# Kernel tuning notes

Hardware: AMD Instinct MI355X
Metric: run time of the kernel (lower is better)

## Reference

```python
import jax, jax.numpy as jnp
import numpy as np

H, KV, D, HID = 32, 2, 128, 4096
SQ, SMAX, CP, L = 1024, 4096, 3072, 4
LAYER_IDX = 0


def setup_inputs() -> dict:
    key = jax.random.key(0)
    ks = jax.random.split(key, 14)
    hidden_states = jax.random.normal(ks[0], (1, HID, 1, SQ), jnp.float32)
    # RoPE tables (values in [-1,1]; layout per forward: cos/sin act on last dim of K,
    # cos_t/sin_t are the transposed tables acting on dim -2 of Q)
    cos = jax.random.uniform(ks[1], (1, 1, SQ, D), jnp.float32, -1.0, 1.0)
    sin = jax.random.uniform(ks[2], (1, 1, SQ, D), jnp.float32, -1.0, 1.0)
    cos_t = jax.random.uniform(ks[3], (1, 1, D, SQ), jnp.float32, -1.0, 1.0)
    sin_t = jax.random.uniform(ks[4], (1, 1, D, SQ), jnp.float32, -1.0, 1.0)
    # causal mask in (kv_pos, q_pos) layout: query q sits at absolute position CP+q
    kv_pos = jnp.arange(SMAX)[:, None]
    q_pos = jnp.arange(SQ)[None, :]
    attention_mask = jnp.where(kv_pos <= CP + q_pos, 0.0, -1e9).astype(jnp.float32)[None, None]
    key_cache = jax.random.normal(ks[5], (L, KV, SMAX, D), jnp.float32)
    value_cache = jax.random.normal(ks[6], (L, KV, SMAX, D), jnp.float32)
    s = 0.02
    wq = jax.random.normal(ks[7], (H * D, HID), jnp.float32) * s
    bq = jax.random.normal(ks[8], (H * D,), jnp.float32) * s
    wk = jax.random.normal(ks[9], (KV * D, HID), jnp.float32) * s
    bk = jax.random.normal(ks[10], (KV * D,), jnp.float32) * s
    wv = jax.random.normal(ks[11], (KV * D, HID), jnp.float32) * s
    bv = jax.random.normal(ks[12], (KV * D,), jnp.float32) * s
    wo = jax.random.normal(ks[13], (HID, H * D), jnp.float32) * s
    return dict(hidden_states=hidden_states, cos=cos, sin=sin, cos_t=cos_t, sin_t=sin_t,
                attention_mask=attention_mask, key_cache=key_cache, value_cache=value_cache,
                wq=wq, bq=bq, wk=wk, bk=bk, wv=wv, bv=bv, wo=wo, cache_position=CP)


def _rotate_half(x, axis):
    x1, x2 = jnp.split(x, 2, axis=axis)
    return jnp.concatenate([-x2, x1], axis=axis)


def reference(hidden_states, cos, sin, cos_t, sin_t, attention_mask,
              key_cache, value_cache, wq, bq, wk, bk, wv, bv, wo, cache_position):
    cp = int(cache_position)
    # 1x1-conv projections == matmul over channel dim; hidden_states (1, HID, 1, SQ)
    q = jnp.einsum('oi,bihs->bohs', wq, hidden_states) + bq[None, :, None, None]
    k = jnp.einsum('oi,bihs->bohs', wk, hidden_states) + bk[None, :, None, None]
    v = jnp.einsum('oi,bihs->bohs', wv, hidden_states) + bv[None, :, None, None]
    q = q.reshape(1, H, D, SQ)                      # (1, H, D, Sq)
    k = k.reshape(1, KV, D, SQ).swapaxes(2, 3)      # (1, KV, Sq, D)
    v = v.reshape(1, KV, D, SQ).swapaxes(2, 3)      # (1, KV, Sq, D)
    # split-half RoPE: q rotated along dim -2 (head_dim axis), k along dim -1
    q = q * cos_t + _rotate_half(q, -2) * sin_t
    k = k * cos + _rotate_half(k, -1) * sin
    # scatter into KV cache at [layer_idx, :, cp:cp+SQ]
    kc = key_cache.at[LAYER_IDX, :, cp:cp + SQ, :].set(k[0])
    vc = value_cache.at[LAYER_IDX, :, cp:cp + SQ, :].set(v[0])
    kl = kc[LAYER_IDX]   # (KV, Smax, D)
    vl = vc[LAYER_IDX]   # (KV, Smax, D)
    qg = q.reshape(KV, H // KV, D, SQ)  # group G=H/KV query heads per kv head
    # K @ Q per kv-head group, softmax over kv positions (axis=2)
    attn = jnp.einsum('ksd,kgdq->kgsq', kl, qg) / jnp.sqrt(jnp.float32(D))
    attn = attn + attention_mask[0]     # broadcast (1, Smax, Sq) over (KV, G, Smax, Sq)
    attn = jax.nn.softmax(attn, axis=2)
    out = jnp.einsum('kgsq,ksd->kgqd', attn, vl)    # (KV, G, Sq, D)
    out = out.reshape(1, H, SQ, D).swapaxes(2, 3).reshape(1, H * D, 1, SQ)
    out = jnp.einsum('oi,bihs->bohs', wo, out)      # (1, HID, 1, Sq)
    return out
```

## Files before the change

### kernel.cpp

```cpp
#include <hip/hip_runtime.h>
#include <stdint.h>

#define H_    32
#define KV_   2
#define D_    128
#define HID_  4096
#define SQ_   1024
#define SMAX_ 4096

typedef unsigned short u16;
typedef __attribute__((ext_vector_type(8))) short bf16x8;
typedef __attribute__((ext_vector_type(8))) unsigned short u16x8;
typedef __attribute__((ext_vector_type(4))) float f32x4;

#define MFMA16(a, b, c) __builtin_amdgcn_mfma_f32_16x16x32_bf16(a, b, c, 0, 0, 0)

__device__ __forceinline__ u16 f2bf(float f) {
  unsigned u = __float_as_uint(f);
  u += 0x7fffu + ((u >> 16) & 1u);
  return (u16)(u >> 16);
}
__device__ __forceinline__ float bf2f(u16 u) {
  return __uint_as_float(((unsigned)u) << 16);
}
__device__ __forceinline__ float exp2_fast(float x) {
  float r;
  asm("v_exp_f32 %0, %1" : "=v"(r) : "v"(x));
  return r;
}
__device__ __forceinline__ unsigned cvt_pk_bf16(float lo, float hi) {
  unsigned r;
  asm("v_cvt_pk_bf16_f32 %0, %1, %2" : "=v"(r) : "v"(lo), "v"(hi));
  return r;
}

__device__ __forceinline__ void gl_lds16(const void* g, void* l) {
  __builtin_amdgcn_global_load_lds(
      (const __attribute__((address_space(1))) unsigned int*)g,
      (__attribute__((address_space(3))) unsigned int*)l, 16, 0, 0);
}

__global__ __launch_bounds__(256) void k_ht(const float* __restrict__ hs,
                                            u16* __restrict__ ht) {
  __shared__ float tl[64][65];
  const int i0 = blockIdx.x << 6, s0 = blockIdx.y << 6;
  const int tid = threadIdx.x;
  {
    const int r = tid >> 2, c = (tid & 3) << 4;
    const float* p = hs + (i0 + r) * SQ_ + s0 + c;
    float4 a = *(const float4*)p;
    float4 b = *(const float4*)(p + 4);
    float4 cc = *(const float4*)(p + 8);
    float4 d = *(const float4*)(p + 12);
    float* q = &tl[r][c];
    q[0] = a.x; q[1] = a.y; q[2] = a.z; q[3] = a.w;
    q[4] = b.x; q[5] = b.y; q[6] = b.z; q[7] = b.w;
    q[8] = cc.x; q[9] = cc.y; q[10] = cc.z; q[11] = cc.w;
    q[12] = d.x; q[13] = d.y; q[14] = d.z; q[15] = d.w;
  }
  __syncthreads();
  {
    const int sr = tid >> 2, c = (tid & 3) << 4;
    u16x8 o0, o1;
#pragma unroll
    for (int j = 0; j < 8; ++j) o0[j] = f2bf(tl[c + j][sr]);
#pragma unroll
    for (int j = 0; j < 8; ++j) o1[j] = f2bf(tl[c + 8 + j][sr]);
    u16* q = ht + (s0 + sr) * HID_ + i0 + c;
    *(u16x8*)q = o0;
    *(u16x8*)(q + 8) = o1;
  }
}

__global__ __launch_bounds__(256) void k_wconv4(const float* __restrict__ s0,
                                                const float* __restrict__ s1,
                                                const float* __restrict__ s2,
                                                const float* __restrict__ s3,
                                                u16* __restrict__ dbase) {
  const int N0 = (H_ * D_ * HID_) / 8;
  const int N1 = (KV_ * D_ * HID_) / 8;
  const int NT = N0 + 2 * N1 + N0;
  const int stride = gridDim.x << 8;
  for (int i = (blockIdx.x << 8) + threadIdx.x; i < NT; i += stride) {
    const float* s;
    int j;
    if (i < N0) { s = s0; j = i; }
    else if (i < N0 + N1) { s = s1; j = i - N0; }
    else if (i < N0 + 2 * N1) { s = s2; j = i - N0 - N1; }
    else { s = s3; j = i - N0 - 2 * N1; }
    const float4 a = ((const float4*)s)[2 * j];
    const float4 b = ((const float4*)s)[2 * j + 1];
    u16x8 o;
    o[0] = f2bf(a.x); o[1] = f2bf(a.y); o[2] = f2bf(a.z); o[3] = f2bf(a.w);
    o[4] = f2bf(b.x); o[5] = f2bf(b.y); o[6] = f2bf(b.z); o[7] = f2bf(b.w);
    ((u16x8*)dbase)[i] = o;
  }
}

template <int OUTMODE, bool SWZ>
__global__ __launch_bounds__(256, 2) void k_gemm_bf(const u16* __restrict__ A,
                                                    const float* __restrict__ bias,
                                                    const u16* __restrict__ B,
                                                    void* __restrict__ Cout,
                                                    const int* __restrict__ cpp,
                                                    int ldc,
                                                    const float* __restrict__ bk2,
                                                    const float* __restrict__ bv2,
                                                    u16* __restrict__ knr2,
                                                    u16* __restrict__ vt2) {
  __shared__ u16 a_t[2][64 * 64];
  __shared__ u16 b_t[2][128 * 64];
  int nx, my;
  if (SWZ) {
    const int bid = blockIdx.x;
    const int xcd = bid & 7, t = bid >> 3;
    nx = t & 7;
    my = ((t >> 3) << 3) | xcd;
  } else {
    nx = blockIdx.x;
    my = blockIdx.y;
  }
  const int n0 = nx << 7, m0 = my << 6;
  const int tid = threadIdx.x, wid = tid >> 6, lane = tid & 63;
  const int l15 = lane & 15, l4 = lane >> 4;
  const int wn = wid << 5;
  const f32x4 z4 = {0.f, 0.f, 0.f, 0.f};
  f32x4 acc[4][2];
#pragma unroll
  for (int i = 0; i < 4; ++i)
#pragma unroll
    for (int j = 0; j < 2; ++j) acc[i][j] = z4;

  const int lr8 = lane >> 3, sl = lane & 7;
  const char* sp[6];
  u16* dp[6];
  int stp[6];
#pragma unroll
  for (int j = 0; j < 6; ++j) {
    const int L = wid * 6 + j;
    const bool isA = (L < 8);
    const int Lr = isA ? L : (L - 8);
    const int row = (Lr << 3) + lr8;
    const int cs = sl ^ (row & 7);
    const size_t grow = isA ? (size_t)(m0 + row) : (size_t)(n0 + row);
    sp[j] = (const char*)((isA ? A : B) + grow * HID_) + (cs << 4);
    dp[j] = (isA ? &a_t[0][0] : &b_t[0][0]) + (Lr << 9);
    stp[j] = isA ? 4096 : 8192;
  }
#define GSTAGE(buf, kt)                                     \
  {                                                         \
    _Pragma("unroll") for (int j = 0; j < 6; ++j)           \
        gl_lds16(sp[j] + ((size_t)(kt) << 7),               \
                 dp[j] + ((buf) ? stp[j] : 0));             \
  }

  GSTAGE(0, 0);
  __syncthreads();
  int cur = 0;
  for (int kt = 0; kt < HID_ / 64; ++kt) {
    if (kt + 1 < HID_ / 64) GSTAGE(cur ^ 1, kt + 1);
#pragma unroll
    for (int kk = 0; kk < 2; ++kk) {
      bf16x8 af[4], bfr[2];
#pragma unroll
      for (int mf = 0; mf < 4; ++mf) {
        const int row = mf * 16 + l15;
        const int slt = ((kk << 2) + l4) ^ (row & 7);
        af[mf] = *(const bf16x8*)((const char*)&a_t[cur][0] + (row << 7) + (slt << 4));
      }
#pragma unroll
      for (int nf = 0; nf < 2; ++nf) {
        const int row = wn + nf * 16 + l15;
        const int slt = ((kk << 2) + l4) ^ (row & 7);
        bfr[nf] = *(const bf16x8*)((const char*)&b_t[cur][0] + (row << 7) + (slt << 4));
      }
#pragma unroll
      for (int nf = 0; nf < 2; ++nf)
#pragma unroll
        for (int mf = 0; mf < 4; ++mf) acc[mf][nf] = MFMA16(af[mf], bfr[nf], acc[mf][nf]);
    }
    __syncthreads();
    cur ^= 1;
  }
#undef GSTAGE

  if (OUTMODE == 3) {
    const int cp = cpp[0];
#pragma unroll
    for (int mf = 0; mf < 4; ++mf) {
#pragma unroll
      for (int r = 0; r < 4; ++r) {
        const int m = m0 + mf * 16 + (l4 << 2) + r;
        float bi;
        u16* dst;
        if (m < 4096) { bi = bias[m]; dst = (u16*)Cout + (size_t)m * SQ_; }
        else if (m < 4352) { bi = bk2[m - 4096]; dst = knr2 + (size_t)(m - 4096) * SQ_; }
        else { bi = bv2[m - 4352]; dst = vt2 + (size_t)(m - 4352) * SMAX_ + cp; }
#pragma unroll
        for (int nf = 0; nf < 2; ++nf) {
          const int n = n0 + wn + nf * 16 + l15;
          dst[n] = f2bf(acc[mf][nf][r] + bi);
        }
      }
    }
  } else {
#pragma unroll
    for (int mf = 0; mf < 4; ++mf) {
#pragma unroll
      for (int r = 0; r < 4; ++r) {
        const int m = m0 + mf * 16 + (l4 << 2) + r;
        const float bi = bias ? bias[m] : 0.f;
#pragma unroll
        for (int nf = 0; nf < 2; ++nf) {
          const int n = n0 + wn + nf * 16 + l15;
          const float v = acc[mf][nf][r] + bi;
          if (OUTMODE == 2)
            ((float*)Cout)[(size_t)m * ldc + n] = v;
          else
            ((u16*)Cout)[(size_t)m * ldc + n] = f2bf(v);
        }
      }
    }
  }
}

template <int OUTMODE>
__global__ __launch_bounds__(256) void k_gemm_f32A(const float* __restrict__ A,
                                                   const float* __restrict__ bias,
                                                   const u16* __restrict__ B,
                                                   void* __restrict__ Cout,
                                                   const int* __restrict__ cpp,
                                                   int ldc) {
  __shared__ u16 a_t[128 * 32];
  __shared__ u16 b_t[128 * 32];
  const int n0 = blockIdx.x << 7, m0 = blockIdx.y << 7;
  const int tid = threadIdx.x;
  const int wid = tid >> 6, lane = tid & 63;
  const int l15 = lane & 15, l4 = lane >> 4;
  const int wm = (wid >> 1) * 64, wn = (wid & 1) * 64;
  const f32x4 z4 = {0.f, 0.f, 0.f, 0.f};
  f32x4 acc[4][4];
#pragma unroll
  for (int i = 0; i < 4; ++i)
#pragma unroll
    for (int j = 0; j < 4; ++j) acc[i][j] = z4;
  const int arow = tid >> 1, ac = (tid & 1) << 4;
  const float* Ap = A + (size_t)(m0 + arow) * HID_ + ac;
  const u16* Bp = B + (size_t)(n0 + arow) * HID_ + ac;
  for (int kt = 0; kt < HID_ / 32; ++kt) {
    float4 f0 = *(const float4*)(Ap);
    float4 f1 = *(const float4*)(Ap + 4);
    float4 f2 = *(const float4*)(Ap + 8);
    float4 f3 = *(const float4*)(Ap + 12);
    uint4 b0 = *(const uint4*)(Bp);
    uint4 b1 = *(const uint4*)(Bp + 8);
    Ap += 32;
    Bp += 32;
    u16x8 ua0, ua1;
    ua0[0] = f2bf(f0.x); ua0[1] = f2bf(f0.y); ua0[2] = f2bf(f0.z); ua0[3] = f2bf(f0.w);
    ua0[4] = f2bf(f1.x); ua0[5] = f2bf(f1.y); ua0[6] = f2bf(f1.z); ua0[7] = f2bf(f1.w);
    ua1[0] = f2bf(f2.x); ua1[1] = f2bf(f2.y); ua1[2] = f2bf(f2.z); ua1[3] = f2bf(f2.w);
    ua1[4] = f2bf(f3.x); ua1[5] = f2bf(f3.y); ua1[6] = f2bf(f3.z); ua1[7] = f2bf(f3.w);
    __syncthreads();
    *(u16x8*)&a_t[arow * 32 + ac] = ua0;
    *(u16x8*)&a_t[arow * 32 + ac + 8] = ua1;
    *(uint4*)&b_t[arow * 32 + ac] = b0;
    *(uint4*)&b_t[arow * 32 + ac + 8] = b1;
    __syncthreads();
    bf16x8 af[4];
#pragma unroll
    for (int mf = 0; mf < 4; ++mf)
      af[mf] = *(const bf16x8*)&a_t[(wm + mf * 16 + l15) * 32 + l4 * 8];
#pragma unroll
    for (int nf = 0; nf < 4; ++nf) {
      bf16x8 bfr = *(const bf16x8*)&b_t[(wn + nf * 16 + l15) * 32 + l4 * 8];
#pragma unroll
      for (int mf = 0; mf < 4; ++mf) acc[mf][nf] = MFMA16(af[mf], bfr, acc[mf][nf]);
    }
  }
  const int coff = (OUTMODE == 1) ? cpp[0] : 0;
#pragma unroll
  for (int mf = 0; mf < 4; ++mf) {
#pragma unroll
    for (int r = 0; r < 4; ++r) {
      const int m = m0 + wm + mf * 16 + l4 * 4 + r;
      const float bi = bias ? bias[m] : 0.f;
#pragma unroll
      for (int nf = 0; nf < 4; ++nf) {
        const int n = n0 + wn + nf * 16 + l15;
        const float v = acc[mf][nf][r] + bi;
        if (OUTMODE == 2)
          ((float*)Cout)[(size_t)m * ldc + n] = v;
        else
          ((u16*)Cout)[(size_t)m * ldc + n + coff] = f2bf(v);
      }
    }
  }
}

__global__ __launch_bounds__(256) void k_rope_q(const u16* __restrict__ qnr,
                                                const float* __restrict__ cost,
                                                const float* __restrict__ sint,
                                                u16* __restrict__ Qr) {
  __shared__ u16 qt[128 * 64];
  __shared__ float ct[128 * 64];
  __shared__ float st[128 * 64];
  const int s0 = blockIdx.x << 6, h = blockIdx.y;
  const int tid = threadIdx.x;
  {
    const int r = tid >> 1, c = (tid & 1) << 5;
    const u16* p = qnr + (h * 128 + r) * SQ_ + s0 + c;
#pragma unroll
    for (int j = 0; j < 4; ++j) *(uint4*)&qt[r * 64 + c + j * 8] = *(const uint4*)(p + j * 8);
    const float* cpr = cost + r * SQ_ + s0 + c;
    const float* spr = sint + r * SQ_ + s0 + c;
#pragma unroll
    for (int j = 0; j < 8; ++j) {
      *(float4*)&ct[r * 64 + c + j * 4] = *(const float4*)(cpr + j * 4);
      *(float4*)&st[r * 64 + c + j * 4] = *(const float4*)(spr + j * 4);
    }
  }
  __syncthreads();
  const int sl = tid >> 2, d0 = (tid & 3) << 5;
  u16* op = Qr + (((h << 10) + s0 + sl) << 7) + d0;
#pragma unroll
  for (int g = 0; g < 4; ++g) {
    u16x8 o;
#pragma unroll
    for (int j = 0; j < 8; ++j) {
      const int d = d0 + g * 8 + j;
      const float v = bf2f(qt[d * 64 + sl]);
      const float vp = bf2f(qt[(d ^ 64) * 64 + sl]);
      const float sgn = (d < 64) ? -1.f : 1.f;
      o[j] = f2bf(v * ct[d * 64 + sl] + sgn * vp * st[d * 64 + sl]);
    }
    *(u16x8*)(op + g * 8) = o;
  }
}

__global__ __launch_bounds__(256) void k_rope_k(const u16* __restrict__ knr,
                                                const float* __restrict__ cosp,
                                                const float* __restrict__ sinp,
                                                const int* __restrict__ cpp,
                                                u16* __restrict__ kful) {
  __shared__ u16 kt_[128 * 64];
  const int s0 = blockIdx.x << 6, kk = blockIdx.y;
  const int cp = cpp[0];
  const int tid = threadIdx.x;
  {
    const int r = tid >> 1, c = (tid & 1) << 5;
    const u16* p = knr + (kk * 128 + r) * SQ_ + s0 + c;
#pragma unroll
    for (int j = 0; j < 4; ++j) *(uint4*)&kt_[r * 64 + c + j * 8] = *(const uint4*)(p + j * 8);
  }
  __syncthreads();
  const int sl = tid >> 2, d0 = (tid & 3) << 5;
  const int s = s0 + sl;
  const float* crow = cosp + s * D_;
  const float* srow = sinp + s * D_;
  u16* op = kful + ((kk * SMAX_ + cp + s) << 7) + d0;
#pragma unroll
  for (int g = 0; g < 4; ++g) {
    u16x8 o;
#pragma unroll
    for (int j = 0; j < 8; ++j) {
      const int d = d0 + g * 8 + j;
      const float v = bf2f(kt_[d * 64 + sl]);
      const float vp = bf2f(kt_[(d ^ 64) * 64 + sl]);
      const float sgn = (d < 64) ? -1.f : 1.f;
      o[j] = f2bf(v * crow[d] + sgn * vp * srow[d]);
    }
    *(u16x8*)(op + g * 8) = o;
  }
}

__global__ __launch_bounds__(256) void k_prefk(const float* __restrict__ kc,
                                               const int* __restrict__ cpp,
                                               u16* __restrict__ kful) {
  const int cp = cpp[0];
  const int idx = (blockIdx.x << 8) + threadIdx.x;
  const int base = idx << 3;
  const int s = (base >> 7) & (SMAX_ - 1);
  if (s >= cp) return;
  const float* p = kc + base;
  float4 a = *(const float4*)p;
  float4 b = *(const float4*)(p + 4);
  u16x8 o;
  o[0] = f2bf(a.x); o[1] = f2bf(a.y); o[2] = f2bf(a.z); o[3] = f2bf(a.w);
  o[4] = f2bf(b.x); o[5] = f2bf(b.y); o[6] = f2bf(b.z); o[7] = f2bf(b.w);
  *(u16x8*)(kful + base) = o;
}

__global__ __launch_bounds__(256) void k_prefvt(const float* __restrict__ vc,
                                                const int* __restrict__ cpp,
                                                u16* __restrict__ vt) {
  const int cp = cpp[0];
  const int s0 = blockIdx.x << 6, d0 = blockIdx.y << 6, kk = blockIdx.z;
  if (s0 >= cp) return;
  __shared__ float tl[64][65];
  const int tid = threadIdx.x;
  {
    const int r = tid >> 2, c = (tid & 3) << 4;
    if (s0 + r < cp) {
      const float* p = vc + ((kk * SMAX_ + s0 + r) << 7) + d0 + c;
#pragma unroll
      for (int j = 0; j < 4; ++j) {
        float4 v = *(const float4*)(p + j * 4);
        tl[r][c + j * 4 + 0] = v.x;
        tl[r][c + j * 4 + 1] = v.y;
        tl[r][c + j * 4 + 2] = v.z;
        tl[r][c + j * 4 + 3] = v.w;
      }
    }
  }
  __syncthreads();
  const int dl = tid >> 2, c = (tid & 3) << 4;
  u16* op = vt + (kk * D_ + d0 + dl) * SMAX_ + s0 + c;
  if (s0 + c + 15 < cp) {
    u16x8 o0, o1;
#pragma unroll
    for (int j = 0; j < 8; ++j) o0[j] = f2bf(tl[c + j][dl]);
#pragma unroll
    for (int j = 0; j < 8; ++j) o1[j] = f2bf(tl[c + 8 + j][dl]);
    *(u16x8*)op = o0;
    *(u16x8*)(op + 8) = o1;
  } else {
#pragma unroll
    for (int j = 0; j < 16; ++j)
      if (s0 + c + j < cp) op[j] = f2bf(tl[c + j][dl]);
  }
}

__device__ __forceinline__ void attn_stageK8(const char* KfB, int kv0, u16* kbuf,
                                             int wid, int lane) {
  const int kcb = (lane & 15) << 4;
#pragma unroll
  for (int j = 0; j < 2; ++j) {
    const int L = (wid << 1) + j;
    const int row = (L << 2) + (lane >> 4);
    gl_lds16(KfB + (((size_t)(kv0 + row)) << 8) + (kcb ^ ((row & 7) << 4)),
             kbuf + (L << 9));
  }
}
__device__ __forceinline__ void attn_stageV8(const char* VtB, int kv0, u16* vbuf,
                                             int wid, int lane) {
  const int vcb = (lane & 7) << 4;
#pragma unroll
  for (int j = 0; j < 2; ++j) {
    const int L = (wid << 1) + j;
    const int row = (L << 3) + (lane >> 3);
    gl_lds16(VtB + ((((size_t)row * SMAX_) + kv0) << 1) + (vcb ^ ((row & 7) << 4)),
             vbuf + (L << 9));
  }
}

template <int SPLIT>
__global__ __launch_bounds__(512, 4) void k_attn(const u16* __restrict__ Q,
                                                 const u16* __restrict__ Kf,
                                                 const u16* __restrict__ Vt,
                                                 const int* __restrict__ cpp,
                                                 u16* __restrict__ Ob,
                                                 float* __restrict__ Opart,
                                                 float* __restrict__ Ml) {
  __shared__ u16 Kb[2][8192];
  __shared__ u16 Vb[2][8192];
  __shared__ u16 Pl[8][1024];
  int h, qb, ch;
  if (SPLIT) {
    const int bid = blockIdx.x;
    const int xcd = bid & 7, s = bid >> 3;
    h = ((xcd >> 2) << 4) | (xcd & 3) | ((s & 3) << 2);
    qb = (s >> 2) & 7;
    ch = s >> 5;
  } else {
    h = blockIdx.x;
    qb = blockIdx.y;
    ch = 0;
  }
  const int cp = cpp[0];
  const int kk = h >> 4;
  const int tid = threadIdx.x, wid = tid >> 6, lane = tid & 63;
  const int l15 = lane & 15, l4 = lane >> 4;
  const int qrow_base = (qb << 7) + (wid << 4);
  char* pl = (char*)&Pl[wid][0];

  bf16x8 aq[4];
#pragma unroll
  for (int ks = 0; ks < 4; ++ks)
    aq[ks] = *(const bf16x8*)&Q[(((size_t)(h << 10) + qrow_base + l15) << 7) + ks * 32 + (l4 << 3)];

  const f32x4 z4 = {0.f, 0.f, 0.f, 0.f};
  f32x4 oacc[8];
  float mrun = -1e30f, lrun = 0.f;
#pragma unroll
  for (int nf = 0; nf < 8; ++nf) oacc[nf] = z4;

  const int ntf0 = ((cp + (qb << 7) + 127) >> 6) + 1;
  const int ntf = ntf0 < (SMAX_ >> 6) ? ntf0 : (SMAX_ >> 6);
  const int t0 = (SPLIT && ch) ? 32 : 0;
  const int t1 = (SPLIT && !ch) ? 32 : ntf;
  const float SC2 = 0.12751879523568785f;

  const char* KfB = (const char*)Kf + ((size_t)kk * SMAX_ << 8);
  const char* VtB = (const char*)Vt + ((size_t)kk << 20);

  attn_stageK8(KfB, t0 << 6, Kb[0], wid, lane);
  attn_stageV8(VtB, t0 << 6, Vb[0], wid, lane);
  __syncthreads();
  int cur = 0;

  for (int kt = t0; kt < t1; ++kt) {
    const int kv0 = kt << 6;
    if (kt + 1 < t1) {
      attn_stageK8(KfB, kv0 + 64, Kb[cur ^ 1], wid, lane);
      attn_stageV8(VtB, kv0 + 64, Vb[cur ^ 1], wid, lane);
    }
    const char* kb = (const char*)Kb[cur];
    const char* vb = (const char*)Vb[cur];
    f32x4 sa[4];
#pragma unroll
    for (int nf = 0; nf < 4; ++nf) sa[nf] = z4;
#pragma unroll
    for (int ks = 0; ks < 4; ++ks) {
#pragma unroll
      for (int nf = 0; nf < 4; ++nf) {
        const int rk = nf * 16 + l15;
        bf16x8 bk = *(const bf16x8*)(kb + (((rk << 8) + (ks << 6) + (l4 << 4)) ^ ((rk & 7) << 4)));
        sa[nf] = MFMA16(bk, aq[ks], sa[nf]);
      }
    }
    const int lim = cp + qrow_base + l15;
    const bool needmask = (kv0 + 63) > (cp + qrow_base);
    float x[4][4];
#pragma unroll
    for (int nf = 0; nf < 4; ++nf)
#pragma unroll
      for (int r = 0; r < 4; ++r) {
        float v = sa[nf][r] * SC2;
        if (needmask && (kv0 + nf * 16 + (l4 << 2) + r > lim)) v = -1e9f;
        x[nf][r] = v;
      }
    float ml = x[0][0];
#pragma unroll
    for (int nf = 0; nf < 4; ++nf)
#pragma unroll
      for (int r = 0; r < 4; ++r) ml = fmaxf(ml, x[nf][r]);
    ml = fmaxf(ml, __shfl_xor(ml, 16));
    ml = fmaxf(ml, __shfl_xor(ml, 32));
    const bool need = !__all(ml <= mrun + 11.54f);
    const float mnew = need ? fmaxf(ml, mrun) : mrun;
    float rs = 0.f;
#pragma unroll
    for (int nf = 0; nf < 4; ++nf) {
      const float p0 = exp2_fast(x[nf][0] - mnew);
      const float p1 = exp2_fast(x[nf][1] - mnew);
      const float p2 = exp2_fast(x[nf][2] - mnew);
      const float p3 = exp2_fast(x[nf][3] - mnew);
      rs += (p0 + p1) + (p2 + p3);
      uint2 w;
      w.x = cvt_pk_bf16(p0, p1);
      w.y = cvt_pk_bf16(p2, p3);
      const unsigned byte = (unsigned)(((l15 << 7) + (nf << 5) + (l4 << 3)) ^ ((l15 & 7) << 4));
      *(uint2*)(pl + byte) = w;
    }
    rs += __shfl_xor(rs, 16);
    rs += __shfl_xor(rs, 32);
    if (need) {
      const float sf = exp2_fast(mrun - mnew);
      lrun = lrun * sf + rs;
      mrun = mnew;
      float sfr[4];
#pragma unroll
      for (int r = 0; r < 4; ++r) sfr[r] = __shfl(sf, (l4 << 2) + r);
#pragma unroll
      for (int nf = 0; nf < 8; ++nf)
#pragma unroll
        for (int r = 0; r < 4; ++r) oacc[nf][r] *= sfr[r];
    } else {
      lrun += rs;
    }
    bf16x8 ap[2];
#pragma unroll
    for (int k2 = 0; k2 < 2; ++k2) {
      const unsigned byte = (unsigned)(((l15 << 7) + (k2 << 6) + (l4 << 4)) ^ ((l15 & 7) << 4));
      ap[k2] = *(const bf16x8*)(pl + byte);
    }
#pragma unroll
    for (int nf = 0; nf < 8; ++nf) {
#pragma unroll
      for (int k2 = 0; k2 < 2; ++k2) {
        const int rv = nf * 16 + l15;
        bf16x8 bv = *(const bf16x8*)(vb + (((rv << 7) + (k2 << 6) + (l4 << 4)) ^ ((rv & 7) << 4)));
        oacc[nf] = MFMA16(ap[k2], bv, oacc[nf]);
      }
    }
    __syncthreads();
    cur ^= 1;
  }

  float lq[4], mq[4];
#pragma unroll
  for (int r = 0; r < 4; ++r) {
    lq[r] = __shfl(lrun, (l4 << 2) + r);
    mq[r] = __shfl(mrun, (l4 << 2) + r);
  }
  if (SPLIT) {
    float* Obase = Opart + ((((size_t)ch << 5) + h) << 17);
#pragma unroll
    for (int r = 0; r < 4; ++r) {
      const int row = qrow_base + (l4 << 2) + r;
      float* op = Obase + ((size_t)row << 7);
#pragma unroll
      for (int nf = 0; nf < 8; ++nf) op[nf * 16 + l15] = oacc[nf][r];
      if (l15 == 0) {
        float* mlp = Ml + ((((((size_t)ch << 5) + h) << 10) + row) << 1);
        mlp[0] = mq[r];
        mlp[1] = lq[r];
      }
    }
  } else {
#pragma unroll
    for (int r = 0; r < 4; ++r) {
      const float inv = 1.f / lq[r];
      const int qrow = qrow_base + (l4 << 2) + r;
#pragma unroll
      for (int nf = 0; nf < 8; ++nf)
        Ob[((size_t)qrow << 12) + (h << 7) + nf * 16 + l15] = f2bf(oacc[nf][r] * inv);
    }
  }
}

__global__ __launch_bounds__(256) void k_merge(const float* __restrict__ Opart,
                                               const float* __restrict__ Ml,
                                               u16* __restrict__ Ob) {
  const int h = blockIdx.x, qb = blockIdx.y;
  const int tid = threadIdx.x;
  const int row = (qb << 6) + (tid >> 2);
  const int d0 = (tid & 3) << 5;
  const size_t r0 = ((size_t)h << 10) + row;
  const size_t r1 = r0 + ((size_t)32 << 10);
  const float m0 = Ml[2 * r0], l0 = Ml[2 * r0 + 1];
  const float m1 = Ml[2 * r1], l1 = Ml[2 * r1 + 1];
  const float mm = fmaxf(m0, m1);
  const float w0 = exp2_fast(m0 - mm), w1 = exp2_fast(m1 - mm);
  const float inv = 1.f / (w0 * l0 + w1 * l1);
  const float a0 = w0 * inv, a1 = w1 * inv;
  const float* p0 = Opart + (r0 << 7) + d0;
  const float* p1 = Opart + (r1 << 7) + d0;
  u16* ob = Ob + (((size_t)row) << 12) + (h << 7) + d0;
#pragma unroll
  for (int g = 0; g < 4; ++g) {
    float4 u = *(const float4*)(p0 + g * 8);
    float4 v = *(const float4*)(p0 + g * 8 + 4);
    float4 x = *(const float4*)(p1 + g * 8);
    float4 y = *(const float4*)(p1 + g * 8 + 4);
    u16x8 o;
    o[0] = f2bf(a0 * u.x + a1 * x.x);
    o[1] = f2bf(a0 * u.y + a1 * x.y);
    o[2] = f2bf(a0 * u.z + a1 * x.z);
    o[3] = f2bf(a0 * u.w + a1 * x.w);
    o[4] = f2bf(a0 * v.x + a1 * y.x);
    o[5] = f2bf(a0 * v.y + a1 * y.y);
    o[6] = f2bf(a0 * v.z + a1 * y.z);
    o[7] = f2bf(a0 * v.w + a1 * y.w);
    *(u16x8*)(ob + g * 8) = o;
  }
}

extern "C" void kernel_launch(void* const* d_in, const int* in_sizes, int n_in,
                              void* d_out, int out_size, void* d_ws, size_t ws_size,
                              hipStream_t stream) {
  const float* hs    = (const float*)d_in[0];
  const float* cosp  = (const float*)d_in[1];
  const float* sinp  = (const float*)d_in[2];
  const float* cost  = (const float*)d_in[3];
  const float* sint  = (const float*)d_in[4];
  const float* kcache = (const float*)d_in[6];
  const float* vcache = (const float*)d_in[7];
  const float* wq = (const float*)d_in[8];
  const float* bq = (const float*)d_in[9];
  const float* wk = (const float*)d_in[10];
  const float* bk = (const float*)d_in[11];
  const float* wv = (const float*)d_in[12];
  const float* bv = (const float*)d_in[13];
  const float* wo = (const float*)d_in[14];
  const int* cpp = (const int*)d_in[15];

  char* ws = (char*)d_ws;
  u16* ht   = (u16*)(ws);
  u16* qnr  = (u16*)(ws + 8388608);
  u16* Qr   = (u16*)(ws + 16777216);
  u16* knr  = (u16*)(ws + 25165824);
  u16* kful = (u16*)(ws + 25690112);
  u16* vt   = (u16*)(ws + 27787264);
  u16* Ob   = (u16*)(ws + 29884416);

  const size_t WOFF  = 38273024;
  const size_t SZ_WQ = (size_t)H_ * D_ * HID_ * 2;
  const size_t SZ_WK = (size_t)KV_ * D_ * HID_ * 2;
  const size_t SZ_WO = (size_t)HID_ * H_ * D_ * 2;
  const size_t OPOFF = WOFF + SZ_WQ + 2 * SZ_WK + SZ_WO;
  const size_t SZ_OP = (size_t)2 * 32 * 1024 * 128 * 4;
  const size_t MLOFF = OPOFF + SZ_OP;
  const size_t SZ_ML = (size_t)2 * 32 * 1024 * 2 * 4;
  const bool pre = ws_size >= OPOFF;
  const bool splitok = pre && ws_size >= MLOFF + SZ_ML;

  k_ht<<<dim3(64, 16), 256, 0, stream>>>(hs, ht);
  if (pre) {
    u16* wqb = (u16*)(ws + WOFF);
    u16* wkb = (u16*)(ws + WOFF + SZ_WQ);
    u16* wvb = (u16*)(ws + WOFF + SZ_WQ + SZ_WK);
    u16* wob = (u16*)(ws + WOFF + SZ_WQ + 2 * SZ_WK);
    float* Opart = (float*)(ws + OPOFF);
    float* Ml    = (float*)(ws + MLOFF);
    k_wconv4<<<2048, 256, 0, stream>>>(wq, wk, wv, wo, wqb);
    k_gemm_bf<3, true><<<576, 256, 0, stream>>>(wqb, bq, ht, (void*)qnr, cpp, SQ_,
                                                bk, bv, knr, vt);
    k_rope_q<<<dim3(16, 32), 256, 0, stream>>>(qnr, cost, sint, Qr);
    k_rope_k<<<dim3(16, 2), 256, 0, stream>>>(knr, cosp, sinp, cpp, kful);
    k_prefk<<<dim3(512), 256, 0, stream>>>(kcache, cpp, kful);
    k_prefvt<<<dim3(64, 2, 2), 256, 0, stream>>>(vcache, cpp, vt);
    if (splitok) {
      k_attn<1><<<512, 512, 0, stream>>>(Qr, kful, vt, cpp, Ob, Opart, Ml);
      k_merge<<<dim3(32, 16), 256, 0, stream>>>(Opart, Ml, Ob);
    } else {
      k_attn<0><<<dim3(32, 8), 512, 0, stream>>>(Qr, kful, vt, cpp, Ob, nullptr, nullptr);
    }
    k_gemm_bf<2, true><<<512, 256, 0, stream>>>(wob, nullptr, Ob, d_out, nullptr, SQ_,
                                                nullptr, nullptr, nullptr, nullptr);
  } else {
    k_gemm_f32A<0><<<dim3(8, 32), 256, 0, stream>>>(wq, bq, ht, (void*)qnr, nullptr, SQ_);
    k_gemm_f32A<0><<<dim3(8, 2), 256, 0, stream>>>(wk, bk, ht, (void*)knr, nullptr, SQ_);
    k_gemm_f32A<1><<<dim3(8, 2), 256, 0, stream>>>(wv, bv, ht, (void*)vt, cpp, SMAX_);
    k_rope_q<<<dim3(16, 32), 256, 0, stream>>>(qnr, cost, sint, Qr);
    k_rope_k<<<dim3(16, 2), 256, 0, stream>>>(knr, cosp, sinp, cpp, kful);
    k_prefk<<<dim3(512), 256, 0, stream>>>(kcache, cpp, kful);
    k_prefvt<<<dim3(64, 2, 2), 256, 0, stream>>>(vcache, cpp, vt);
    k_attn<0><<<dim3(32, 8), 512, 0, stream>>>(Qr, kful, vt, cpp, Ob, nullptr, nullptr);
    k_gemm_f32A<2><<<dim3(8, 32), 256, 0, stream>>>(wo, nullptr, Ob, d_out, nullptr, SQ_);
  }
  (void)in_sizes; (void)n_in; (void)out_size; (void)ws_size;
}
```

Before: 274.1 us.

## Fuse fp32-to-bf16 weight conversion into GEMM A-tile loads, drop separate convert pass

```diff
diff --git a/kernel.cpp b/kernel.cpp
--- a/kernel.cpp
+++ b/kernel.cpp
@@ -72,42 +72,18 @@
   }
 }
 
-__global__ __launch_bounds__(256) void k_wconv4(const float* __restrict__ s0,
-                                                const float* __restrict__ s1,
-                                                const float* __restrict__ s2,
-                                                const float* __restrict__ s3,
-                                                u16* __restrict__ dbase) {
-  const int N0 = (H_ * D_ * HID_) / 8;
-  const int N1 = (KV_ * D_ * HID_) / 8;
-  const int NT = N0 + 2 * N1 + N0;
-  const int stride = gridDim.x << 8;
-  for (int i = (blockIdx.x << 8) + threadIdx.x; i < NT; i += stride) {
-    const float* s;
-    int j;
-    if (i < N0) { s = s0; j = i; }
-    else if (i < N0 + N1) { s = s1; j = i - N0; }
-    else if (i < N0 + 2 * N1) { s = s2; j = i - N0 - N1; }
-    else { s = s3; j = i - N0 - 2 * N1; }
-    const float4 a = ((const float4*)s)[2 * j];
-    const float4 b = ((const float4*)s)[2 * j + 1];
-    u16x8 o;
-    o[0] = f2bf(a.x); o[1] = f2bf(a.y); o[2] = f2bf(a.z); o[3] = f2bf(a.w);
-    o[4] = f2bf(b.x); o[5] = f2bf(b.y); o[6] = f2bf(b.z); o[7] = f2bf(b.w);
-    ((u16x8*)dbase)[i] = o;
-  }
-}
-
 template <int OUTMODE, bool SWZ>
-__global__ __launch_bounds__(256, 2) void k_gemm_bf(const u16* __restrict__ A,
-                                                    const float* __restrict__ bias,
-                                                    const u16* __restrict__ B,
-                                                    void* __restrict__ Cout,
-                                                    const int* __restrict__ cpp,
-                                                    int ldc,
-                                                    const float* __restrict__ bk2,
-                                                    const float* __restrict__ bv2,
-                                                    u16* __restrict__ knr2,
-                                                    u16* __restrict__ vt2) {
+__global__ __launch_bounds__(256, 2) void k_gemm(const float* __restrict__ A0,
+                                                 const float* __restrict__ A1,
+                                                 const float* __restrict__ A2,
+                                                 const float* __restrict__ bias,
+                                                 const u16* __restrict__ B,
+                                                 void* __restrict__ Cout,
+                                                 const int* __restrict__ cpp,
+                                                 const float* __restrict__ bk2,
+                                                 const float* __restrict__ bv2,
+                                                 u16* __restrict__ knr2,
+                                                 u16* __restrict__ vt2) {
   __shared__ u16 a_t[2][64 * 64];
   __shared__ u16 b_t[2][128 * 64];
   int nx, my;
@@ -131,34 +107,77 @@
 #pragma unroll
     for (int j = 0; j < 2; ++j) acc[i][j] = z4;
 
-  const int lr8 = lane >> 3, sl = lane & 7;
-  const char* sp[6];
-  u16* dp[6];
-  int stp[6];
-#pragma unroll
-  for (int j = 0; j < 6; ++j) {
-    const int L = wid * 6 + j;
-    const bool isA = (L < 8);
-    const int Lr = isA ? L : (L - 8);
-    const int row = (Lr << 3) + lr8;
-    const int cs = sl ^ (row & 7);
-    const size_t grow = isA ? (size_t)(m0 + row) : (size_t)(n0 + row);
-    sp[j] = (const char*)((isA ? A : B) + grow * HID_) + (cs << 4);
-    dp[j] = (isA ? &a_t[0][0] : &b_t[0][0]) + (Lr << 9);
-    stp[j] = isA ? 4096 : 8192;
-  }
-#define GSTAGE(buf, kt)                                     \
+  const int ar0 = tid >> 3;
+  const int ls = (tid & 7) ^ (ar0 & 7);
+  const int g0r = m0 + ar0, g1r = g0r + 32;
+  const float* Ap0;
+  const float* Ap1;
+  if (OUTMODE == 3) {
+    Ap0 = (g0r < 4096) ? A0 + (size_t)g0r * HID_
+        : (g0r < 4352) ? A1 + (size_t)(g0r - 4096) * HID_
+                       : A2 + (size_t)(g0r - 4352) * HID_;
+    Ap1 = (g1r < 4096) ? A0 + (size_t)g1r * HID_
+        : (g1r < 4352) ? A1 + (size_t)(g1r - 4096) * HID_
+                       : A2 + (size_t)(g1r - 4352) * HID_;
+  } else {
+    Ap0 = A0 + (size_t)g0r * HID_;
+    Ap1 = A0 + (size_t)g1r * HID_;
+  }
+  Ap0 += (ls << 3);
+  Ap1 += (ls << 3);
+
+  const char* spB[4];
+  u16* dpB[4];
+#pragma unroll
+  for (int j = 0; j < 4; ++j) {
+    const int L = (wid << 2) + j;
+    const int row = (L << 3) + (lane >> 3);
+    const int cs = (lane & 7) ^ (row & 7);
+    spB[j] = (const char*)(B + (size_t)(n0 + row) * HID_) + (cs << 4);
+    dpB[j] = &b_t[0][0] + (L << 9);
+  }
+#define GSTAGEB(buf, kt)                                    \
   {                                                         \
-    _Pragma("unroll") for (int j = 0; j < 6; ++j)           \
-        gl_lds16(sp[j] + ((size_t)(kt) << 7),               \
-                 dp[j] + ((buf) ? stp[j] : 0));             \
-  }
-
-  GSTAGE(0, 0);
+    _Pragma("unroll") for (int j = 0; j < 4; ++j)           \
+        gl_lds16(spB[j] + ((size_t)(kt) << 7),              \
+                 dpB[j] + ((buf) ? 8192 : 0));              \
+  }
+#define LOADA(kt)                                           \
+  {                                                         \
+    const int co = (kt) << 6;                               \
+    ra0 = *(const float4*)(Ap0 + co);                       \
+    ra1 = *(const float4*)(Ap0 + co + 4);                   \
+    ra2 = *(const float4*)(Ap1 + co);                       \
+    ra3 = *(const float4*)(Ap1 + co + 4);                   \
+  }
+#define WRITEA(buf)                                         \
+  {                                                         \
+    uint4 w0, w1;                                           \
+    w0.x = cvt_pk_bf16(ra0.x, ra0.y);                       \
+    w0.y = cvt_pk_bf16(ra0.z, ra0.w);                       \
+    w0.z = cvt_pk_bf16(ra1.x, ra1.y);                       \
+    w0.w = cvt_pk_bf16(ra1.z, ra1.w);                       \
+    w1.x = cvt_pk_bf16(ra2.x, ra2.y);                       \
+    w1.y = cvt_pk_bf16(ra2.z, ra2.w);                       \
+    w1.z = cvt_pk_bf16(ra3.x, ra3.y);                       \
+    w1.w = cvt_pk_bf16(ra3.z, ra3.w);                       \
+    *(uint4*)&a_t[buf][(tid << 3)] = w0;                    \
+    *(uint4*)&a_t[buf][2048 + (tid << 3)] = w1;             \
+  }
+
+  float4 ra0, ra1, ra2, ra3;
+  LOADA(0);
+  GSTAGEB(0, 0);
+  WRITEA(0);
   __syncthreads();
   int cur = 0;
-  for (int kt = 0; kt < HID_ / 64; ++kt) {
-    if (kt + 1 < HID_ / 64) GSTAGE(cur ^ 1, kt + 1);
+  const int NT = HID_ / 64;
+  for (int kt = 0; kt < NT; ++kt) {
+    const bool pf = (kt + 1) < NT;
+    if (pf) {
+      LOADA(kt + 1);
+      GSTAGEB(cur ^ 1, kt + 1);
+    }
 #pragma unroll
     for (int kk = 0; kk < 2; ++kk) {
       bf16x8 af[4], bfr[2];
@@ -179,10 +198,13 @@
 #pragma unroll
         for (int mf = 0; mf < 4; ++mf) acc[mf][nf] = MFMA16(af[mf], bfr[nf], acc[mf][nf]);
     }
+    if (pf) WRITEA(cur ^ 1);
     __syncthreads();
     cur ^= 1;
   }
-#undef GSTAGE
+#undef GSTAGEB
+#undef LOADA
+#undef WRITEA
 
   if (OUTMODE == 3) {
     const int cp = cpp[0];
@@ -209,90 +231,11 @@
 #pragma unroll
       for (int r = 0; r < 4; ++r) {
         const int m = m0 + mf * 16 + (l4 << 2) + r;
-        const float bi = bias ? bias[m] : 0.f;
 #pragma unroll
         for (int nf = 0; nf < 2; ++nf) {
           const int n = n0 + wn + nf * 16 + l15;
-          const float v = acc[mf][nf][r] + bi;
-          if (OUTMODE == 2)
-            ((float*)Cout)[(size_t)m * ldc + n] = v;
-          else
-            ((u16*)Cout)[(size_t)m * ldc + n] = f2bf(v);
+          ((float*)Cout)[(size_t)m * SQ_ + n] = acc[mf][nf][r];
         }
-      }
-    }
-  }
-}
-
-template <int OUTMODE>
-__global__ __launch_bounds__(256) void k_gemm_f32A(const float* __restrict__ A,
-                                                   const float* __restrict__ bias,
-                                                   const u16* __restrict__ B,
-                                                   void* __restrict__ Cout,
-                                                   const int* __restrict__ cpp,
-                                                   int ldc) {
-  __shared__ u16 a_t[128 * 32];
-  __shared__ u16 b_t[128 * 32];
-  const int n0 = blockIdx.x << 7, m0 = blockIdx.y << 7;
-  const int tid = threadIdx.x;
-  const int wid = tid >> 6, lane = tid & 63;
-  const int l15 = lane & 15, l4 = lane >> 4;
-  const int wm = (wid >> 1) * 64, wn = (wid & 1) * 64;
-  const f32x4 z4 = {0.f, 0.f, 0.f, 0.f};
-  f32x4 acc[4][4];
-#pragma unroll
-  for (int i = 0; i < 4; ++i)
-#pragma unroll
-    for (int j = 0; j < 4; ++j) acc[i][j] = z4;
-  const int arow = tid >> 1, ac = (tid & 1) << 4;
-  const float* Ap = A + (size_t)(m0 + arow) * HID_ + ac;
-  const u16* Bp = B + (size_t)(n0 + arow) * HID_ + ac;
-  for (int kt = 0; kt < HID_ / 32; ++kt) {
-    float4 f0 = *(const float4*)(Ap);
-    float4 f1 = *(const float4*)(Ap + 4);
-    float4 f2 = *(const float4*)(Ap + 8);
-    float4 f3 = *(const float4*)(Ap + 12);
-    uint4 b0 = *(const uint4*)(Bp);
-    uint4 b1 = *(const uint4*)(Bp + 8);
-    Ap += 32;
-    Bp += 32;
-    u16x8 ua0, ua1;
-    ua0[0] = f2bf(f0.x); ua0[1] = f2bf(f0.y); ua0[2] = f2bf(f0.z); ua0[3] = f2bf(f0.w);
-    ua0[4] = f2bf(f1.x); ua0[5] = f2bf(f1.y); ua0[6] = f2bf(f1.z); ua0[7] = f2bf(f1.w);
-    ua1[0] = f2bf(f2.x); ua1[1] = f2bf(f2.y); ua1[2] = f2bf(f2.z); ua1[3] = f2bf(f2.w);
-    ua1[4] = f2bf(f3.x); ua1[5] = f2bf(f3.y); ua1[6] = f2bf(f3.z); ua1[7] = f2bf(f3.w);
-    __syncthreads();
-    *(u16x8*)&a_t[arow * 32 + ac] = ua0;
-    *(u16x8*)&a_t[arow * 32 + ac + 8] = ua1;
-    *(uint4*)&b_t[arow * 32 + ac] = b0;
-    *(uint4*)&b_t[arow * 32 + ac + 8] = b1;
-    __syncthreads();
-    bf16x8 af[4];
-#pragma unroll
-    for (int mf = 0; mf < 4; ++mf)
-      af[mf] = *(const bf16x8*)&a_t[(wm + mf * 16 + l15) * 32 + l4 * 8];
-#pragma unroll
-    for (int nf = 0; nf < 4; ++nf) {
-      bf16x8 bfr = *(const bf16x8*)&b_t[(wn + nf * 16 + l15) * 32 + l4 * 8];
-#pragma unroll
-      for (int mf = 0; mf < 4; ++mf) acc[mf][nf] = MFMA16(af[mf], bfr, acc[mf][nf]);
-    }
-  }
-  const int coff = (OUTMODE == 1) ? cpp[0] : 0;
-#pragma unroll
-  for (int mf = 0; mf < 4; ++mf) {
-#pragma unroll
-    for (int r = 0; r < 4; ++r) {
-      const int m = m0 + wm + mf * 16 + l4 * 4 + r;
-      const float bi = bias ? bias[m] : 0.f;
-#pragma unroll
-      for (int nf = 0; nf < 4; ++nf) {
-        const int n = n0 + wn + nf * 16 + l15;
-        const float v = acc[mf][nf][r] + bi;
-        if (OUTMODE == 2)
-          ((float*)Cout)[(size_t)m * ldc + n] = v;
-        else
-          ((u16*)Cout)[(size_t)m * ldc + n + coff] = f2bf(v);
       }
     }
   }
@@ -530,32 +473,30 @@
       }
     }
     const int lim = cp + qrow_base + l15;
-    const bool needmask = (kv0 + 63) > (cp + qrow_base);
-    float x[4][4];
+    if ((kv0 + 63) > (cp + qrow_base)) {
+#pragma unroll
+      for (int nf = 0; nf < 4; ++nf)
+#pragma unroll
+        for (int r = 0; r < 4; ++r)
+          if (kv0 + nf * 16 + (l4 << 2) + r > lim) sa[nf][r] = -8e9f;
+    }
+    float t4[4];
 #pragma unroll
     for (int nf = 0; nf < 4; ++nf)
-#pragma unroll
-      for (int r = 0; r < 4; ++r) {
-        float v = sa[nf][r] * SC2;
-        if (needmask && (kv0 + nf * 16 + (l4 << 2) + r > lim)) v = -1e9f;
-        x[nf][r] = v;
-      }
-    float ml = x[0][0];
-#pragma unroll
-    for (int nf = 0; nf < 4; ++nf)
-#pragma unroll
-      for (int r = 0; r < 4; ++r) ml = fmaxf(ml, x[nf][r]);
+      t4[nf] = fmaxf(fmaxf(sa[nf][0], sa[nf][1]), fmaxf(sa[nf][2], sa[nf][3]));
+    float ml = fmaxf(fmaxf(t4[0], t4[1]), fmaxf(t4[2], t4[3])) * SC2;
     ml = fmaxf(ml, __shfl_xor(ml, 16));
     ml = fmaxf(ml, __shfl_xor(ml, 32));
     const bool need = !__all(ml <= mrun + 11.54f);
     const float mnew = need ? fmaxf(ml, mrun) : mrun;
+    const float nm = -mnew;
     float rs = 0.f;
 #pragma unroll
     for (int nf = 0; nf < 4; ++nf) {
-      const float p0 = exp2_fast(x[nf][0] - mnew);
-      const float p1 = exp2_fast(x[nf][1] - mnew);
-      const float p2 = exp2_fast(x[nf][2] - mnew);
-      const float p3 = exp2_fast(x[nf][3] - mnew);
+      const float p0 = exp2_fast(fmaf(sa[nf][0], SC2, nm));
+      const float p1 = exp2_fast(fmaf(sa[nf][1], SC2, nm));
+      const float p2 = exp2_fast(fmaf(sa[nf][2], SC2, nm));
+      const float p3 = exp2_fast(fmaf(sa[nf][3], SC2, nm));
       rs += (p0 + p1) + (p2 + p3);
       uint2 w;
       w.x = cvt_pk_bf16(p0, p1);
@@ -695,50 +636,28 @@
   u16* vt   = (u16*)(ws + 27787264);
   u16* Ob   = (u16*)(ws + 29884416);
 
-  const size_t WOFF  = 38273024;
-  const size_t SZ_WQ = (size_t)H_ * D_ * HID_ * 2;
-  const size_t SZ_WK = (size_t)KV_ * D_ * HID_ * 2;
-  const size_t SZ_WO = (size_t)HID_ * H_ * D_ * 2;
-  const size_t OPOFF = WOFF + SZ_WQ + 2 * SZ_WK + SZ_WO;
+  const size_t OPOFF = 113770496;
   const size_t SZ_OP = (size_t)2 * 32 * 1024 * 128 * 4;
   const size_t MLOFF = OPOFF + SZ_OP;
   const size_t SZ_ML = (size_t)2 * 32 * 1024 * 2 * 4;
-  const bool pre = ws_size >= OPOFF;
-  const bool splitok = pre && ws_size >= MLOFF + SZ_ML;
+  const bool splitok = ws_size >= MLOFF + SZ_ML;
+  float* Opart = (float*)(ws + OPOFF);
+  float* Ml    = (float*)(ws + MLOFF);
 
   k_ht<<<dim3(64, 16), 256, 0, stream>>>(hs, ht);
-  if (pre) {
-    u16* wqb = (u16*)(ws + WOFF);
-    u16* wkb = (u16*)(ws + WOFF + SZ_WQ);
-    u16* wvb = (u16*)(ws + WOFF + SZ_WQ + SZ_WK);
-    u16* wob = (u16*)(ws + WOFF + SZ_WQ + 2 * SZ_WK);
-    float* Opart = (float*)(ws + OPOFF);
-    float* Ml    = (float*)(ws + MLOFF);
-    k_wconv4<<<2048, 256, 0, stream>>>(wq, wk, wv, wo, wqb);
-    k_gemm_bf<3, true><<<576, 256, 0, stream>>>(wqb, bq, ht, (void*)qnr, cpp, SQ_,
-                                                bk, bv, knr, vt);
-    k_rope_q<<<dim3(16, 32), 256, 0, stream>>>(qnr, cost, sint, Qr);
-    k_rope_k<<<dim3(16, 2), 256, 0, stream>>>(knr, cosp, sinp, cpp, kful);
-    k_prefk<<<dim3(512), 256, 0, stream>>>(kcache, cpp, kful);
-    k_prefvt<<<dim3(64, 2, 2), 256, 0, stream>>>(vcache, cpp, vt);
-    if (splitok) {
-      k_attn<1><<<512, 512, 0, stream>>>(Qr, kful, vt, cpp, Ob, Opart, Ml);
-      k_merge<<<dim3(32, 16), 256, 0, stream>>>(Opart, Ml, Ob);
-    } else {
-      k_attn<0><<<dim3(32, 8), 512, 0, stream>>>(Qr, kful, vt, cpp, Ob, nullptr, nullptr);
-    }
-    k_gemm_bf<2, true><<<512, 256, 0, stream>>>(wob, nullptr, Ob, d_out, nullptr, SQ_,
-                                                nullptr, nullptr, nullptr, nullptr);
+  k_gemm<3, true><<<576, 256, 0, stream>>>(wq, wk, wv, bq, ht, (void*)qnr, cpp,
+                                           bk, bv, knr, vt);
+  k_rope_q<<<dim3(16, 32), 256, 0, stream>>>(qnr, cost, sint, Qr);
+  k_rope_k<<<dim3(16, 2), 256, 0, stream>>>(knr, cosp, sinp, cpp, kful);
+  k_prefk<<<dim3(512), 256, 0, stream>>>(kcache, cpp, kful);
+  k_prefvt<<<dim3(64, 2, 2), 256, 0, stream>>>(vcache, cpp, vt);
+  if (splitok) {
+    k_attn<1><<<512, 512, 0, stream>>>(Qr, kful, vt, cpp, Ob, Opart, Ml);
+    k_merge<<<dim3(32, 16), 256, 0, stream>>>(Opart, Ml, Ob);
   } else {
-    k_gemm_f32A<0><<<dim3(8, 32), 256, 0, stream>>>(wq, bq, ht, (void*)qnr, nullptr, SQ_);
-    k_gemm_f32A<0><<<dim3(8, 2), 256, 0, stream>>>(wk, bk, ht, (void*)knr, nullptr, SQ_);
-    k_gemm_f32A<1><<<dim3(8, 2), 256, 0, stream>>>(wv, bv, ht, (void*)vt, cpp, SMAX_);
-    k_rope_q<<<dim3(16, 32), 256, 0, stream>>>(qnr, cost, sint, Qr);
-    k_rope_k<<<dim3(16, 2), 256, 0, stream>>>(knr, cosp, sinp, cpp, kful);
-    k_prefk<<<dim3(512), 256, 0, stream>>>(kcache, cpp, kful);
-    k_prefvt<<<dim3(64, 2, 2), 256, 0, stream>>>(vcache, cpp, vt);
     k_attn<0><<<dim3(32, 8), 512, 0, stream>>>(Qr, kful, vt, cpp, Ob, nullptr, nullptr);
-    k_gemm_f32A<2><<<dim3(8, 32), 256, 0, stream>>>(wo, nullptr, Ob, d_out, nullptr, SQ_);
-  }
+  }
+  k_gemm<2, true><<<512, 256, 0, stream>>>(wo, nullptr, nullptr, nullptr, Ob,
+                                           d_out, cpp, nullptr, nullptr, nullptr, nullptr);
   (void)in_sizes; (void)n_in; (void)out_size; (void)ws_size;
 }
```

Result: slower. 386.2 us (+40.9%).
